# Optimization experiments

Hardware: AMD Instinct MI355X
Metric: run time of the kernel (lower is better)

Reference implementation:

```python
import jax, jax.numpy as jnp
import numpy as np

N = 20000
NNBR = 64
MESH = (64, 64, 64)
ORDER = 4          # B-spline interpolation order
ALPHA = 0.35       # Ewald splitting parameter (1/Angstrom)
BOX = 73.68        # cubic box edge (Angstrom)
KE = 14.399645478425668  # Coulomb constant, eV*Angstrom/e^2


def _Mn(x, n):
    """Cardinal B-spline M_n(x), support [0, n]."""
    if n == 2:
        return jnp.maximum(0.0, 1.0 - jnp.abs(x - 1.0))
    return (x * _Mn(x, n - 1) + (n - x) * _Mn(x - 1.0, n - 1)) / (n - 1)


def _bspline_fac(K):
    """|b(m)|^-2 ... i.e. 1/|Euler spline denominator|^2 per mesh dim."""
    m = jnp.arange(K, dtype=jnp.float32)
    k = jnp.arange(ORDER - 1, dtype=jnp.float32)
    Mv = _Mn(k + 1.0, ORDER)                       # M_n(1..n-1)
    phase = 2.0 * jnp.pi * m[:, None] * k[None, :] / K
    dre = jnp.sum(Mv * jnp.cos(phase), axis=1)
    dim = jnp.sum(Mv * jnp.sin(phase), axis=1)
    return 1.0 / (dre * dre + dim * dim)


def _pme_energy(positions, charges, cell, nbr, shifts):
    n = positions.shape[0]
    # ---------------- real-space short-range sum ----------------
    i_idx = jnp.arange(n)[:, None]
    valid = (nbr >= 0) & ~((nbr == i_idx) & jnp.all(shifts == 0, axis=-1))
    j = jnp.where(nbr >= 0, nbr, 0)
    rvec = positions[j] + shifts.astype(positions.dtype) @ cell - positions[:, None, :]
    r2 = jnp.sum(rvec * rvec, axis=-1)
    r = jnp.sqrt(jnp.where(valid, r2, 1.0))
    qq = charges[:, None] * charges[j]
    e_real = 0.5 * jnp.sum(jnp.where(valid, qq * jax.scipy.special.erfc(ALPHA * r) / r, 0.0))
    # ---------------- B-spline charge spreading ----------------
    Kx, Ky, Kz = MESH
    frac = positions @ jnp.linalg.inv(cell)        # cell rows = lattice vectors
    u = frac * jnp.array(MESH, dtype=positions.dtype)
    base = jnp.floor(u)
    t = u - base                                   # in [0, 1)
    basei = base.astype(jnp.int32)
    offs = jnp.arange(ORDER)
    wx = _Mn(t[:, 0:1] + offs, ORDER)              # [N, ORDER]
    wy = _Mn(t[:, 1:2] + offs, ORDER)
    wz = _Mn(t[:, 2:3] + offs, ORDER)
    ix = (basei[:, 0:1] - offs) % Kx
    iy = (basei[:, 1:2] - offs) % Ky
    iz = (basei[:, 2:3] - offs) % Kz
    W = (charges[:, None] * wx)[:, :, None, None] * wy[:, None, :, None] * wz[:, None, None, :]
    IDX = (ix[:, :, None, None] * Ky + iy[:, None, :, None]) * Kz + iz[:, None, None, :]
    mesh = jnp.zeros(Kx * Ky * Kz, positions.dtype).at[IDX.reshape(-1)].add(W.reshape(-1)).reshape(MESH)
    # ---------------- reciprocal-space FFT convolution ----------------
    Q = jnp.fft.fftn(mesh)
    Brec = 2.0 * jnp.pi * jnp.linalg.inv(cell).T   # rows are reciprocal vectors
    mx = (jnp.fft.fftfreq(Kx) * Kx).astype(positions.dtype)
    my = (jnp.fft.fftfreq(Ky) * Ky).astype(positions.dtype)
    mz = (jnp.fft.fftfreq(Kz) * Kz).astype(positions.dtype)
    kvec = (mx[:, None, None, None] * Brec[0] + my[None, :, None, None] * Brec[1]
            + mz[None, None, :, None] * Brec[2])
    k2 = jnp.sum(kvec * kvec, axis=-1)
    a2 = ALPHA * ALPHA
    kern = jnp.where(k2 > 0, jnp.exp(-k2 / (4.0 * a2)) / jnp.where(k2 > 0, k2, 1.0), 0.0)
    C = _bspline_fac(Kx)[:, None, None] * _bspline_fac(Ky)[None, :, None] * _bspline_fac(Kz)[None, None, :]
    vol = jnp.abs(jnp.linalg.det(cell))
    e_rec = (2.0 * jnp.pi / vol) * jnp.sum(kern * C * (Q.real ** 2 + Q.imag ** 2))
    # ---------------- self + neutralizing background ----------------
    qtot = jnp.sum(charges)
    e_self = -(ALPHA / jnp.sqrt(jnp.pi)) * jnp.sum(charges * charges)
    e_bg = -(jnp.pi / (2.0 * a2 * vol)) * qtot * qtot
    return e_real + e_rec + e_self + e_bg


def setup_inputs() -> dict:
    key = jax.random.key(0)
    k1, k2, k3 = jax.random.split(key, 3)
    positions = jax.random.uniform(k1, (N, 3), jnp.float32) * BOX
    q = jax.random.normal(k2, (N,), jnp.float32)
    q = q - jnp.mean(q)  # neutral system
    cell = BOX * jnp.eye(3, dtype=jnp.float32)
    nbr = jax.random.randint(k3, (N, NNBR), 0, N, jnp.int32)
    shifts = jnp.zeros((N, NNBR, 3), jnp.int32)
    return {"positions": positions, "node_charges": q, "cell": cell,
            "neighbor_matrix": nbr, "neighbor_shifts": shifts}


def reference(positions, node_charges, cell, neighbor_matrix, neighbor_shifts):
    def e_strain(pos, q, c, eps):
        F = jnp.eye(3, dtype=pos.dtype) + eps
        return _pme_energy(pos @ F, q, c @ F, neighbor_matrix, neighbor_shifts)

    eps0 = jnp.zeros((3, 3), positions.dtype)
    e, (g_pos, g_eps) = jax.value_and_grad(e_strain, argnums=(0, 3))(
        positions, node_charges, cell, eps0)
    vol = jnp.abs(jnp.linalg.det(cell))
    energies = e.reshape(1) * KE
    forces = -g_pos * KE
    virial = -0.5 * (g_eps + g_eps.T) * KE
    stresses = (virial / vol)[None]
    return energies, forces, stresses
```

## Files before the change

kernel.cpp:

```cpp
#include <hip/hip_runtime.h>
#include <math.h>

#define NATOM 20000
#define NNBR  64
#define KM    64
#define KM3   (KM*KM*KM)
#define NPAIR (NATOM*NNBR)

#define ALPHA_C 0.35f
#define KE_C    14.399645478425668f
#define TWO_OVER_SQRTPI 1.1283791670955126f
#define TWOPI_F 6.2831853071795864f
#define PI_F    3.14159265358979f
#define RC2     661.2244898f

#define WS_RE    0
#define WS_IM    (KM3)
#define WS_MESH  (2*KM3)
#define WS_GJ    (3*KM3)
#define WS_PART  (3*KM3 + 3*NATOM)
#define WS_FI    (WS_PART + 1024)
#define WS_POSQ  (WS_FI + 3*NATOM)
#define WS_NBS   (WS_POSQ + 4*NATOM)
#define ZERO_LEN (KM3 + 3*NATOM + 1024)

__device__ __forceinline__ float M2f(float x){ return fmaxf(0.f, 1.f - fabsf(x - 1.f)); }
__device__ __forceinline__ float M3f(float x){ return (x*M2f(x) + (3.f-x)*M2f(x-1.f)) * 0.5f; }
__device__ __forceinline__ float M4f(float x){ return (x*M3f(x) + (4.f-x)*M3f(x-1.f)) * (1.f/3.f); }

__device__ __forceinline__ float wsum64(float v){
#pragma unroll
  for(int off=32; off>0; off>>=1) v += __shfl_xor(v, off, 64);
  return v;
}

__device__ __forceinline__ float hinv9(const float* __restrict__ cell, float* h){
  float m00=cell[0],m01=cell[1],m02=cell[2];
  float m10=cell[3],m11=cell[4],m12=cell[5];
  float m20=cell[6],m21=cell[7],m22=cell[8];
  float det = m00*(m11*m22-m12*m21) - m01*(m10*m22-m12*m20) + m02*(m10*m21-m11*m20);
  float id = 1.f/det;
  h[0]=(m11*m22-m12*m21)*id; h[1]=(m02*m21-m01*m22)*id; h[2]=(m01*m12-m02*m11)*id;
  h[3]=(m12*m20-m10*m22)*id; h[4]=(m00*m22-m02*m20)*id; h[5]=(m02*m10-m00*m12)*id;
  h[6]=(m10*m21-m11*m20)*id; h[7]=(m01*m20-m00*m21)*id; h[8]=(m00*m11-m01*m10)*id;
  return fabsf(det);
}

__device__ __forceinline__ void fill_tw(int t, float* twr, float* twi){
  if(t < 64){
    float ss, cc; sincosf((TWOPI_F/64.f)*(float)t, &ss, &cc);
    twr[t] = cc; twi[t] = -ss;
  }
}

__device__ __forceinline__ void fft64t(float& xr, float& xi, int lane,
                                       const float* __restrict__ twr,
                                       const float* __restrict__ twi, float sgn){
#pragma unroll
  for(int k=0;k<6;k++){
    int half = 32 >> k;
    float or_ = __shfl_xor(xr, half, 64);
    float oi_ = __shfl_xor(xi, half, 64);
    bool hi = (lane & half) != 0;
    float sr = hi ? (or_ - xr) : (xr + or_);
    float si = hi ? (oi_ - xi) : (xi + oi_);
    int e = (lane & (half-1)) << k;
    float wr2 = hi ? twr[e] : 1.f;
    float wi2 = hi ? sgn*twi[e] : 0.f;
    xr = sr*wr2 - si*wi2;
    xi = sr*wi2 + si*wr2;
  }
  int rev = __brev((unsigned)lane) >> 26;
  xr = __shfl(xr, rev, 64);
  xi = __shfl(xi, rev, 64);
}

__global__ __launch_bounds__(256) void init_kernel(
    const float* __restrict__ pos, const float* __restrict__ q,
    const int* __restrict__ nbr, const int* __restrict__ shifts,
    float* __restrict__ zbase, float4* __restrict__ posq, int* __restrict__ nbs){
  int t = blockIdx.x*256 + threadIdx.x;
  if(t < ZERO_LEN) zbase[t] = 0.f;
  if(t < NATOM)
    posq[t] = make_float4(pos[3*t], pos[3*t+1], pos[3*t+2], q[t]);
  if(t < NPAIR){
    int j = nbr[t];
    int sx=shifts[3*t], sy=shifts[3*t+1], sz=shifts[3*t+2];
    int v;
    if(j < 0) v = -1;
    else v = (j & 0x7FFF) | ((sx+8)&15)<<15 | ((sy+8)&15)<<19 | ((sz+8)&15)<<23;
    nbs[t] = v;
  }
}

__global__ __launch_bounds__(256) void realspread_kernel(
    const float4* __restrict__ posq, const int* __restrict__ nbs,
    const float* __restrict__ cell,
    float* __restrict__ fi, float* __restrict__ gj, float* __restrict__ part,
    float* __restrict__ mesh){
  int lane = threadIdx.x & 63;
  int wid  = blockIdx.x*4 + (threadIdx.x>>6);
  float c0=cell[0],c1=cell[1],c2=cell[2];
  float c3=cell[3],c4=cell[4],c5=cell[5];
  float c6=cell[6],c7=cell[7],c8=cell[8];
  float h[9]; hinv9(cell, h);
  int la = lane>>4, lb = (lane>>2)&3, lc = lane&3;
  float e=0.f, vxx=0.f,vyy=0.f,vzz=0.f,vxy=0.f,vxz=0.f,vyz=0.f;
#pragma unroll
  for(int it=0; it<4; ++it){
    int i = wid*4 + it;
    float4 pi4 = posq[i];
    int v = nbs[i*NNBR + lane];
    {
      float u0=(pi4.x*h[0]+pi4.y*h[3]+pi4.z*h[6])*(float)KM;
      float u1=(pi4.x*h[1]+pi4.y*h[4]+pi4.z*h[7])*(float)KM;
      float u2=(pi4.x*h[2]+pi4.y*h[5]+pi4.z*h[8])*(float)KM;
      float b0=floorf(u0), b1=floorf(u1), b2=floorf(u2);
      float t0=u0-b0, t1=u1-b1, t2=u2-b2;
      int i0=(int)b0, i1=(int)b1, i2=(int)b2;
      float w = pi4.w * M4f(t0+(float)la) * M4f(t1+(float)lb) * M4f(t2+(float)lc);
      int ix=(i0-la+256)&63, iy=(i1-lb+256)&63, iz=(i2-lc+256)&63;
      unsafeAtomicAdd(&mesh[(ix*KM + iy)*KM + iz], w);
    }
    int j = v & 0x7FFF;
    int sx=((v>>15)&15)-8, sy=((v>>19)&15)-8, sz=((v>>23)&15)-8;
    bool self = (j==i) && (sx==0) && (sy==0) && (sz==0);
    float s=0.f, rx=0.f, ry=0.f, rz=0.f;
    if(v>=0 && !self){
      float4 pj = posq[j];
      rx = pj.x - pi4.x + sx*c0 + sy*c3 + sz*c6;
      ry = pj.y - pi4.y + sx*c1 + sy*c4 + sz*c7;
      rz = pj.z - pi4.z + sx*c2 + sy*c5 + sz*c8;
      float r2 = rx*rx + ry*ry + rz*rz;
      if(r2 > 0.f && r2 < RC2){
        float r = sqrtf(r2);
        float ar = ALPHA_C * r;
        float qq = pi4.w * pj.w;
        float ef = erfcf(ar);
        float ex = expf(-ar*ar);
        float ir = 1.f/r;
        e += 0.5f*qq*ef*ir;
        s  = 0.5f*qq*(ef + TWO_OVER_SQRTPI*ar*ex)*ir*ir*ir;
      }
    }
    float gx = s*rx, gy = s*ry, gz = s*rz;
    if(s != 0.f){
      unsafeAtomicAdd(&gj[3*j+0], -gx);
      unsafeAtomicAdd(&gj[3*j+1], -gy);
      unsafeAtomicAdd(&gj[3*j+2], -gz);
    }
    vxx -= s*rx*rx; vyy -= s*ry*ry; vzz -= s*rz*rz;
    vxy -= s*rx*ry; vxz -= s*rx*rz; vyz -= s*ry*rz;
    float tgx = wsum64(gx), tgy = wsum64(gy), tgz = wsum64(gz);
    if(lane==0){ fi[3*i]=tgx; fi[3*i+1]=tgy; fi[3*i+2]=tgz; }
  }
  e   = wsum64(e);
  vxx = wsum64(vxx); vyy = wsum64(vyy); vzz = wsum64(vzz);
  vxy = wsum64(vxy); vxz = wsum64(vxz); vyz = wsum64(vyz);
  if(lane==0){
    float* slot = part + (wid & 63)*16;
    unsafeAtomicAdd(&slot[0], e);
    unsafeAtomicAdd(&slot[1], vxx); unsafeAtomicAdd(&slot[2], vyy); unsafeAtomicAdd(&slot[3], vzz);
    unsafeAtomicAdd(&slot[4], vxy); unsafeAtomicAdd(&slot[5], vxz); unsafeAtomicAdd(&slot[6], vyz);
  }
}

__global__ __launch_bounds__(256) void fftZF(const float* __restrict__ mesh,
                                             float* __restrict__ re, float* __restrict__ im){
  __shared__ float twr[64], twi[64];
  int t = threadIdx.x, lane = t&63;
  fill_tw(t, twr, twi);
  __syncthreads();
  int idx = blockIdx.x*256 + t;
  float xr = mesh[idx], xi = 0.f;
  fft64t(xr, xi, lane, twr, twi, 1.f);
  re[idx]=xr; im[idx]=xi;
}

__global__ __launch_bounds__(256) void fftZI(float* __restrict__ re, const float* __restrict__ im){
  __shared__ float twr[64], twi[64];
  int t = threadIdx.x, lane = t&63;
  fill_tw(t, twr, twi);
  __syncthreads();
  int idx = blockIdx.x*256 + t;
  float xr = re[idx], xi = im[idx];
  fft64t(xr, xi, lane, twr, twi, -1.f);
  re[idx]=xr;
}

__global__ __launch_bounds__(256) void fftY(float* __restrict__ re, float* __restrict__ im,
                                            float sgn){
  __shared__ float lr[64][17], li[64][17], twr[64], twi[64];
  int t = threadIdx.x, lane = t&63, w = t>>6;
  fill_tw(t, twr, twi);
  int x = blockIdx.x>>2, z0 = (blockIdx.x&3)*16;
  int off = x*4096 + z0;
#pragma unroll
  for(int k=0;k<4;k++){
    int e = k*256 + t; int y = e>>4, zz = e&15;
    lr[y][zz] = re[off + y*64 + zz];
    li[y][zz] = im[off + y*64 + zz];
  }
  __syncthreads();
#pragma unroll
  for(int qq=0; qq<4; qq++){
    int zz = w*4 + qq;
    float xr = lr[lane][zz], xi = li[lane][zz];
    fft64t(xr, xi, lane, twr, twi, sgn);
    lr[lane][zz] = xr; li[lane][zz] = xi;
  }
  __syncthreads();
#pragma unroll
  for(int k=0;k<4;k++){
    int e = k*256 + t; int y = e>>4, zz = e&15;
    re[off + y*64 + zz] = lr[y][zz];
    im[off + y*64 + zz] = li[y][zz];
  }
}

__global__ __launch_bounds__(256) void fftB(float* __restrict__ re, float* __restrict__ im,
                                            const float* __restrict__ cell,
                                            float* __restrict__ part){
  __shared__ float lr[64][17], li[64][17], cf[64], twr[64], twi[64];
  int t = threadIdx.x, lane = t&63, w = t>>6;
  int y = blockIdx.x>>2, z0 = (blockIdx.x&3)*16;
  float h[9]; hinv9(cell, h);
  fill_tw(t, twr, twi);
  if(t < 64){
    float p1 = TWOPI_F*(float)t/64.f;
    float s1,c1_,s2,c2_; sincosf(p1,&s1,&c1_); sincosf(2.f*p1,&s2,&c2_);
    float dre = (1.f/6.f) + (2.f/3.f)*c1_ + (1.f/6.f)*c2_;
    float dim = (2.f/3.f)*s1 + (1.f/6.f)*s2;
    cf[t] = 1.f/(dre*dre + dim*dim);
  }
  float* rp = re + y*64 + z0;
  float* ip = im + y*64 + z0;
#pragma unroll
  for(int k=0;k<4;k++){
    int e = k*256 + t; int xI = e>>4, zz = e&15;
    lr[xI][zz] = rp[xI*4096 + zz];
    li[xI][zz] = ip[xI*4096 + zz];
  }
  __syncthreads();
  const float inv4a2 = 1.f/(4.f*ALPHA_C*ALPHA_C);
  float my_f = (float)((y<32)? y : y-64);
  float sE=0.f, v0=0.f,v1=0.f,v2=0.f,v3=0.f,v4=0.f,v5=0.f;
#pragma unroll
  for(int qq=0; qq<4; qq++){
    int zz = w*4 + qq; int z = z0 + zz;
    float xr = lr[lane][zz], xi = li[lane][zz];
    fft64t(xr, xi, lane, twr, twi, 1.f);
    int mx = lane, mz = z;
    float fx = (float)((mx<32)? mx : mx-64);
    float fz = (float)((mz<32)? mz : mz-64);
    float kx = TWOPI_F*(fx*h[0] + my_f*h[1] + fz*h[2]);
    float ky = TWOPI_F*(fx*h[3] + my_f*h[4] + fz*h[5]);
    float kz = TWOPI_F*(fx*h[6] + my_f*h[7] + fz*h[8]);
    float k2 = kx*kx + ky*ky + kz*kz;
    float wk = 0.f;
    if(k2 > 0.f){
      float kern = expf(-k2*inv4a2)/k2;
      wk = kern * cf[mx]*cf[y]*cf[z];
      float q2 = xr*xr + xi*xi;
      sE += wk*q2;
      float fac = wk*q2*(inv4a2 + 1.f/k2)*2.f;
      v0 += fac*kx*kx; v1 += fac*ky*ky; v2 += fac*kz*kz;
      v3 += fac*kx*ky; v4 += fac*kx*kz; v5 += fac*ky*kz;
    }
    lr[lane][zz] = wk*xr; li[lane][zz] = wk*xi;
  }
  __syncthreads();
#pragma unroll
  for(int k=0;k<4;k++){
    int e = k*256 + t; int xI = e>>4, zz = e&15;
    rp[xI*4096 + zz] = lr[xI][zz];
    ip[xI*4096 + zz] = li[xI][zz];
  }
  sE = wsum64(sE);
  v0 = wsum64(v0); v1 = wsum64(v1); v2 = wsum64(v2);
  v3 = wsum64(v3); v4 = wsum64(v4); v5 = wsum64(v5);
  if(lane==0){
    float* slot = part + (((blockIdx.x<<2)|w)&63)*16;
    unsafeAtomicAdd(&slot[7],  sE);
    unsafeAtomicAdd(&slot[8],  v0); unsafeAtomicAdd(&slot[9],  v1);
    unsafeAtomicAdd(&slot[10], v2); unsafeAtomicAdd(&slot[11], v3);
    unsafeAtomicAdd(&slot[12], v4); unsafeAtomicAdd(&slot[13], v5);
  }
}

__global__ __launch_bounds__(256) void fftC(float* __restrict__ re, float* __restrict__ im){
  __shared__ float lr[64][17], li[64][17], twr[64], twi[64];
  int t = threadIdx.x, lane = t&63, w = t>>6;
  fill_tw(t, twr, twi);
  int y = blockIdx.x>>2, z0 = (blockIdx.x&3)*16;
  float* rp = re + y*64 + z0;
  float* ip = im + y*64 + z0;
#pragma unroll
  for(int k=0;k<4;k++){
    int e = k*256 + t; int xI = e>>4, zz = e&15;
    lr[xI][zz] = rp[xI*4096 + zz];
    li[xI][zz] = ip[xI*4096 + zz];
  }
  __syncthreads();
#pragma unroll
  for(int qq=0; qq<4; qq++){
    int zz = w*4 + qq;
    float xr = lr[lane][zz], xi = li[lane][zz];
    fft64t(xr, xi, lane, twr, twi, -1.f);
    lr[lane][zz] = xr; li[lane][zz] = xi;
  }
  __syncthreads();
#pragma unroll
  for(int k=0;k<4;k++){
    int e = k*256 + t; int xI = e>>4, zz = e&15;
    rp[xI*4096 + zz] = lr[xI][zz];
    ip[xI*4096 + zz] = li[xI][zz];
  }
}

__global__ __launch_bounds__(256) void gather_kernel(
    const float4* __restrict__ posq, const float* __restrict__ cell,
    const float* __restrict__ phi,
    const float* __restrict__ fi, const float* __restrict__ gj,
    const float* __restrict__ part, float* __restrict__ out){
  __shared__ float sa[256], sb[256], facc[16];
  int wid  = blockIdx.x*4 + (threadIdx.x>>6);
  int lane = threadIdx.x & 63;
  float h[9]; float V = hinv9(cell, h);
  float4 pq = posq[wid];
  float u0=(pq.x*h[0]+pq.y*h[3]+pq.z*h[6])*(float)KM;
  float u1=(pq.x*h[1]+pq.y*h[4]+pq.z*h[7])*(float)KM;
  float u2=(pq.x*h[2]+pq.y*h[5]+pq.z*h[8])*(float)KM;
  float b0=floorf(u0), b1=floorf(u1), b2=floorf(u2);
  float t0=u0-b0, t1=u1-b1, t2=u2-b2;
  int i0=(int)b0, i1=(int)b1, i2=(int)b2;
  int a = lane>>4, b = (lane>>2)&3, c = lane&3;
  float fa=(float)a, fb=(float)b, fc=(float)c;
  float wxa=M4f(t0+fa), wyb=M4f(t1+fb), wzc=M4f(t2+fc);
  float dxa=M3f(t0+fa)-M3f(t0+fa-1.f);
  float dyb=M3f(t1+fb)-M3f(t1+fb-1.f);
  float dzc=M3f(t2+fc)-M3f(t2+fc-1.f);
  int ix=(i0-a+256)&63, iy=(i1-b+256)&63, iz=(i2-c+256)&63;
  float p = phi[(ix*KM + iy)*KM + iz];
  float Sx = wsum64(p*dxa*wyb*wzc);
  float Sy = wsum64(p*wxa*dyb*wzc);
  float Sz = wsum64(p*wxa*wyb*dzc);
  if(lane==0){
    float scale = pq.w * (2.f*TWOPI_F/V) * (float)KM;
    float g0 = scale*(Sx*h[0] + Sy*h[1] + Sz*h[2]);
    float g1 = scale*(Sx*h[3] + Sy*h[4] + Sz*h[5]);
    float g2 = scale*(Sx*h[6] + Sy*h[7] + Sz*h[8]);
    out[1+3*wid+0] = -KE_C*(fi[3*wid+0] + gj[3*wid+0] + g0);
    out[1+3*wid+1] = -KE_C*(fi[3*wid+1] + gj[3*wid+1] + g1);
    out[1+3*wid+2] = -KE_C*(fi[3*wid+2] + gj[3*wid+2] + g2);
  }
  if(blockIdx.x==0){
    int t = threadIdx.x;
    float qa=0.f, qb=0.f;
    for(int i=t;i<NATOM;i+=256){ float qv=posq[i].w; qa+=qv; qb+=qv*qv; }
    sa[t]=qa; sb[t]=qb; __syncthreads();
    for(int off=128; off>0; off>>=1){
      if(t<off){ sa[t]+=sa[t+off]; sb[t]+=sb[t+off]; } __syncthreads();
    }
    if(t<14){ float s=0.f; for(int sl=0;sl<64;sl++) s+=part[sl*16+t]; facc[t]=s; }
    __syncthreads();
    if(t==0){
      float qtot = sa[0], sumq2 = sb[0];
      float a2 = ALPHA_C*ALPHA_C;
      float pref = TWOPI_F/V;
      float e_real = facc[0];
      float e_rec  = pref*facc[7];
      float e_self = -(ALPHA_C/sqrtf(PI_F))*sumq2;
      float e_bg   = -(PI_F/(2.f*a2*V))*qtot*qtot;
      out[0] = (e_real + e_rec + e_self + e_bg)*KE_C;
      float gxx = facc[1] + pref*facc[8]  - e_rec - e_bg;
      float gyy = facc[2] + pref*facc[9]  - e_rec - e_bg;
      float gzz = facc[3] + pref*facc[10] - e_rec - e_bg;
      float gxy = facc[4] + pref*facc[11];
      float gxz = facc[5] + pref*facc[12];
      float gyz = facc[6] + pref*facc[13];
      float cc = -KE_C/V;
      float* st = out + 1 + 3*NATOM;
      st[0]=cc*gxx; st[4]=cc*gyy; st[8]=cc*gzz;
      st[1]=cc*gxy; st[3]=cc*gxy;
      st[2]=cc*gxz; st[6]=cc*gxz;
      st[5]=cc*gyz; st[7]=cc*gyz;
    }
  }
}

extern "C" void kernel_launch(void* const* d_in, const int* in_sizes, int n_in,
                              void* d_out, int out_size, void* d_ws, size_t ws_size,
                              hipStream_t stream) {
  const float* pos  = (const float*)d_in[0];
  const float* q    = (const float*)d_in[1];
  const float* cell = (const float*)d_in[2];
  const int* nbr    = (const int*)d_in[3];
  const int* shifts = (const int*)d_in[4];
  float* out = (float*)d_out;
  float* ws  = (float*)d_ws;
  float*  bufRe = ws + WS_RE;
  float*  bufIm = ws + WS_IM;
  float*  mesh  = ws + WS_MESH;
  float*  gj    = ws + WS_GJ;
  float*  part  = ws + WS_PART;
  float*  fi    = ws + WS_FI;
  float4* posq  = (float4*)(ws + WS_POSQ);
  int*    nbs   = (int*)(ws + WS_NBS);

  init_kernel<<<(NPAIR+255)/256,256,0,stream>>>(pos, q, nbr, shifts, mesh, posq, nbs);
  realspread_kernel<<<1250,256,0,stream>>>(posq, nbs, cell, fi, gj, part, mesh);
  fftZF<<<1024,256,0,stream>>>(mesh, bufRe, bufIm);
  fftY <<< 256,256,0,stream>>>(bufRe, bufIm, 1.f);
  fftB <<< 256,256,0,stream>>>(bufRe, bufIm, cell, part);
  fftC <<< 256,256,0,stream>>>(bufRe, bufIm);
  fftY <<< 256,256,0,stream>>>(bufRe, bufIm, -1.f);
  fftZI<<<1024,256,0,stream>>>(bufRe, bufIm);
  gather_kernel<<<5000,256,0,stream>>>(posq, cell, bufRe, fi, gj, part, out);
}
```

Before: 189.6 us.

## Fuse FFT stages into one cooperative kernel and split spreading from real-space pass

The six separate FFT and convolution launches are merged into a single cooperative kernel of 256 blocks, with grid-wide syncs between the Z, Y, X, and inverse stages. This removes several kernel launch gaps. The charge spreading moves out of the real-space kernel into its own 5000-block kernel with one atom per wavefront, so it no longer shares the real-space pair loop's per-iteration structure. In exchange, the Z-direction FFT now runs on only 256 blocks, each doing four passes, instead of 1024 blocks. It also adds grid-sync overhead and one extra launch for spreading.

```diff
diff --git a/kernel.cpp b/kernel.cpp
--- a/kernel.cpp
+++ b/kernel.cpp
@@ -1,5 +1,8 @@
 #include <hip/hip_runtime.h>
+#include <hip/hip_cooperative_groups.h>
 #include <math.h>
+
+namespace cg = cooperative_groups;
 
 #define NATOM 20000
 #define NNBR  64
@@ -93,35 +96,21 @@
   }
 }
 
-__global__ __launch_bounds__(256) void realspread_kernel(
+__global__ __launch_bounds__(256) void real_kernel(
     const float4* __restrict__ posq, const int* __restrict__ nbs,
     const float* __restrict__ cell,
-    float* __restrict__ fi, float* __restrict__ gj, float* __restrict__ part,
-    float* __restrict__ mesh){
+    float* __restrict__ fi, float* __restrict__ gj, float* __restrict__ part){
   int lane = threadIdx.x & 63;
   int wid  = blockIdx.x*4 + (threadIdx.x>>6);
   float c0=cell[0],c1=cell[1],c2=cell[2];
   float c3=cell[3],c4=cell[4],c5=cell[5];
   float c6=cell[6],c7=cell[7],c8=cell[8];
-  float h[9]; hinv9(cell, h);
-  int la = lane>>4, lb = (lane>>2)&3, lc = lane&3;
   float e=0.f, vxx=0.f,vyy=0.f,vzz=0.f,vxy=0.f,vxz=0.f,vyz=0.f;
 #pragma unroll
   for(int it=0; it<4; ++it){
     int i = wid*4 + it;
     float4 pi4 = posq[i];
     int v = nbs[i*NNBR + lane];
-    {
-      float u0=(pi4.x*h[0]+pi4.y*h[3]+pi4.z*h[6])*(float)KM;
-      float u1=(pi4.x*h[1]+pi4.y*h[4]+pi4.z*h[7])*(float)KM;
-      float u2=(pi4.x*h[2]+pi4.y*h[5]+pi4.z*h[8])*(float)KM;
-      float b0=floorf(u0), b1=floorf(u1), b2=floorf(u2);
-      float t0=u0-b0, t1=u1-b1, t2=u2-b2;
-      int i0=(int)b0, i1=(int)b1, i2=(int)b2;
-      float w = pi4.w * M4f(t0+(float)la) * M4f(t1+(float)lb) * M4f(t2+(float)lc);
-      int ix=(i0-la+256)&63, iy=(i1-lb+256)&63, iz=(i2-lc+256)&63;
-      unsafeAtomicAdd(&mesh[(ix*KM + iy)*KM + iz], w);
-    }
     int j = v & 0x7FFF;
     int sx=((v>>15)&15)-8, sy=((v>>19)&15)-8, sz=((v>>23)&15)-8;
     bool self = (j==i) && (sx==0) && (sy==0) && (sz==0);
@@ -165,66 +154,33 @@
   }
 }
 
-__global__ __launch_bounds__(256) void fftZF(const float* __restrict__ mesh,
-                                             float* __restrict__ re, float* __restrict__ im){
-  __shared__ float twr[64], twi[64];
-  int t = threadIdx.x, lane = t&63;
-  fill_tw(t, twr, twi);
-  __syncthreads();
-  int idx = blockIdx.x*256 + t;
-  float xr = mesh[idx], xi = 0.f;
-  fft64t(xr, xi, lane, twr, twi, 1.f);
-  re[idx]=xr; im[idx]=xi;
-}
-
-__global__ __launch_bounds__(256) void fftZI(float* __restrict__ re, const float* __restrict__ im){
-  __shared__ float twr[64], twi[64];
-  int t = threadIdx.x, lane = t&63;
-  fill_tw(t, twr, twi);
-  __syncthreads();
-  int idx = blockIdx.x*256 + t;
-  float xr = re[idx], xi = im[idx];
-  fft64t(xr, xi, lane, twr, twi, -1.f);
-  re[idx]=xr;
-}
-
-__global__ __launch_bounds__(256) void fftY(float* __restrict__ re, float* __restrict__ im,
-                                            float sgn){
-  __shared__ float lr[64][17], li[64][17], twr[64], twi[64];
+__global__ __launch_bounds__(256) void spread_kernel(
+    const float4* __restrict__ posq, const float* __restrict__ cell,
+    float* __restrict__ mesh){
+  int wid  = blockIdx.x*4 + (threadIdx.x>>6);
+  int lane = threadIdx.x & 63;
+  float h[9]; hinv9(cell, h);
+  float4 pq = posq[wid];
+  float u0=(pq.x*h[0]+pq.y*h[3]+pq.z*h[6])*(float)KM;
+  float u1=(pq.x*h[1]+pq.y*h[4]+pq.z*h[7])*(float)KM;
+  float u2=(pq.x*h[2]+pq.y*h[5]+pq.z*h[8])*(float)KM;
+  float b0=floorf(u0), b1=floorf(u1), b2=floorf(u2);
+  float t0=u0-b0, t1=u1-b1, t2=u2-b2;
+  int i0=(int)b0, i1=(int)b1, i2=(int)b2;
+  int a = lane>>4, b = (lane>>2)&3, c = lane&3;
+  float w = pq.w * M4f(t0+(float)a) * M4f(t1+(float)b) * M4f(t2+(float)c);
+  int ix=(i0-a+256)&63, iy=(i1-b+256)&63, iz=(i2-c+256)&63;
+  unsafeAtomicAdd(&mesh[(ix*KM + iy)*KM + iz], w);
+}
+
+__global__ __launch_bounds__(256) void fftAll(
+    float* __restrict__ re, float* __restrict__ im,
+    const float* __restrict__ mesh, const float* __restrict__ cell,
+    float* __restrict__ part){
+  cg::grid_group grid = cg::this_grid();
+  __shared__ float lr[64][17], li[64][17], twr[64], twi[64], cf[64];
   int t = threadIdx.x, lane = t&63, w = t>>6;
-  fill_tw(t, twr, twi);
-  int x = blockIdx.x>>2, z0 = (blockIdx.x&3)*16;
-  int off = x*4096 + z0;
-#pragma unroll
-  for(int k=0;k<4;k++){
-    int e = k*256 + t; int y = e>>4, zz = e&15;
-    lr[y][zz] = re[off + y*64 + zz];
-    li[y][zz] = im[off + y*64 + zz];
-  }
-  __syncthreads();
-#pragma unroll
-  for(int qq=0; qq<4; qq++){
-    int zz = w*4 + qq;
-    float xr = lr[lane][zz], xi = li[lane][zz];
-    fft64t(xr, xi, lane, twr, twi, sgn);
-    lr[lane][zz] = xr; li[lane][zz] = xi;
-  }
-  __syncthreads();
-#pragma unroll
-  for(int k=0;k<4;k++){
-    int e = k*256 + t; int y = e>>4, zz = e&15;
-    re[off + y*64 + zz] = lr[y][zz];
-    im[off + y*64 + zz] = li[y][zz];
-  }
-}
-
-__global__ __launch_bounds__(256) void fftB(float* __restrict__ re, float* __restrict__ im,
-                                            const float* __restrict__ cell,
-                                            float* __restrict__ part){
-  __shared__ float lr[64][17], li[64][17], cf[64], twr[64], twi[64];
-  int t = threadIdx.x, lane = t&63, w = t>>6;
-  int y = blockIdx.x>>2, z0 = (blockIdx.x&3)*16;
-  float h[9]; hinv9(cell, h);
+  int blk = blockIdx.x;
   fill_tw(t, twr, twi);
   if(t < 64){
     float p1 = TWOPI_F*(float)t/64.f;
@@ -233,88 +189,164 @@
     float dim = (2.f/3.f)*s1 + (1.f/6.f)*s2;
     cf[t] = 1.f/(dre*dre + dim*dim);
   }
-  float* rp = re + y*64 + z0;
-  float* ip = im + y*64 + z0;
+  __syncthreads();
+
 #pragma unroll
   for(int k=0;k<4;k++){
-    int e = k*256 + t; int xI = e>>4, zz = e&15;
-    lr[xI][zz] = rp[xI*4096 + zz];
-    li[xI][zz] = ip[xI*4096 + zz];
-  }
-  __syncthreads();
-  const float inv4a2 = 1.f/(4.f*ALPHA_C*ALPHA_C);
-  float my_f = (float)((y<32)? y : y-64);
-  float sE=0.f, v0=0.f,v1=0.f,v2=0.f,v3=0.f,v4=0.f,v5=0.f;
-#pragma unroll
-  for(int qq=0; qq<4; qq++){
-    int zz = w*4 + qq; int z = z0 + zz;
-    float xr = lr[lane][zz], xi = li[lane][zz];
+    int idx = blk*1024 + k*256 + t;
+    float xr = mesh[idx], xi = 0.f;
     fft64t(xr, xi, lane, twr, twi, 1.f);
-    int mx = lane, mz = z;
-    float fx = (float)((mx<32)? mx : mx-64);
-    float fz = (float)((mz<32)? mz : mz-64);
-    float kx = TWOPI_F*(fx*h[0] + my_f*h[1] + fz*h[2]);
-    float ky = TWOPI_F*(fx*h[3] + my_f*h[4] + fz*h[5]);
-    float kz = TWOPI_F*(fx*h[6] + my_f*h[7] + fz*h[8]);
-    float k2 = kx*kx + ky*ky + kz*kz;
-    float wk = 0.f;
-    if(k2 > 0.f){
-      float kern = expf(-k2*inv4a2)/k2;
-      wk = kern * cf[mx]*cf[y]*cf[z];
-      float q2 = xr*xr + xi*xi;
-      sE += wk*q2;
-      float fac = wk*q2*(inv4a2 + 1.f/k2)*2.f;
-      v0 += fac*kx*kx; v1 += fac*ky*ky; v2 += fac*kz*kz;
-      v3 += fac*kx*ky; v4 += fac*kx*kz; v5 += fac*ky*kz;
-    }
-    lr[lane][zz] = wk*xr; li[lane][zz] = wk*xi;
-  }
-  __syncthreads();
+    re[idx]=xr; im[idx]=xi;
+  }
+  grid.sync();
+
+  {
+    int x = blk>>2, z0 = (blk&3)*16;
+    int off = x*4096 + z0;
+#pragma unroll
+    for(int k=0;k<4;k++){
+      int e2 = k*256 + t; int y = e2>>4, zz = e2&15;
+      lr[y][zz] = re[off + y*64 + zz];
+      li[y][zz] = im[off + y*64 + zz];
+    }
+    __syncthreads();
+#pragma unroll
+    for(int qq=0; qq<4; qq++){
+      int zz = w*4 + qq;
+      float xr = lr[lane][zz], xi = li[lane][zz];
+      fft64t(xr, xi, lane, twr, twi, 1.f);
+      lr[lane][zz] = xr; li[lane][zz] = xi;
+    }
+    __syncthreads();
+#pragma unroll
+    for(int k=0;k<4;k++){
+      int e2 = k*256 + t; int y = e2>>4, zz = e2&15;
+      re[off + y*64 + zz] = lr[y][zz];
+      im[off + y*64 + zz] = li[y][zz];
+    }
+  }
+  grid.sync();
+
+  {
+    int y = blk>>2, z0 = (blk&3)*16;
+    float h[9]; hinv9(cell, h);
+    float* rp = re + y*64 + z0;
+    float* ip = im + y*64 + z0;
+#pragma unroll
+    for(int k=0;k<4;k++){
+      int e2 = k*256 + t; int xI = e2>>4, zz = e2&15;
+      lr[xI][zz] = rp[xI*4096 + zz];
+      li[xI][zz] = ip[xI*4096 + zz];
+    }
+    __syncthreads();
+    const float inv4a2 = 1.f/(4.f*ALPHA_C*ALPHA_C);
+    float my_f = (float)((y<32)? y : y-64);
+    float sE=0.f, v0=0.f,v1=0.f,v2=0.f,v3=0.f,v4=0.f,v5=0.f;
+#pragma unroll
+    for(int qq=0; qq<4; qq++){
+      int zz = w*4 + qq; int z = z0 + zz;
+      float xr = lr[lane][zz], xi = li[lane][zz];
+      fft64t(xr, xi, lane, twr, twi, 1.f);
+      int mx = lane, mz = z;
+      float fx = (float)((mx<32)? mx : mx-64);
+      float fz = (float)((mz<32)? mz : mz-64);
+      float kx = TWOPI_F*(fx*h[0] + my_f*h[1] + fz*h[2]);
+      float ky = TWOPI_F*(fx*h[3] + my_f*h[4] + fz*h[5]);
+      float kz = TWOPI_F*(fx*h[6] + my_f*h[7] + fz*h[8]);
+      float k2 = kx*kx + ky*ky + kz*kz;
+      float wk = 0.f;
+      if(k2 > 0.f){
+        float kern = expf(-k2*inv4a2)/k2;
+        wk = kern * cf[mx]*cf[y]*cf[z];
+        float q2 = xr*xr + xi*xi;
+        sE += wk*q2;
+        float fac = wk*q2*(inv4a2 + 1.f/k2)*2.f;
+        v0 += fac*kx*kx; v1 += fac*ky*ky; v2 += fac*kz*kz;
+        v3 += fac*kx*ky; v4 += fac*kx*kz; v5 += fac*ky*kz;
+      }
+      lr[lane][zz] = wk*xr; li[lane][zz] = wk*xi;
+    }
+    __syncthreads();
+#pragma unroll
+    for(int k=0;k<4;k++){
+      int e2 = k*256 + t; int xI = e2>>4, zz = e2&15;
+      rp[xI*4096 + zz] = lr[xI][zz];
+      ip[xI*4096 + zz] = li[xI][zz];
+    }
+    sE = wsum64(sE);
+    v0 = wsum64(v0); v1 = wsum64(v1); v2 = wsum64(v2);
+    v3 = wsum64(v3); v4 = wsum64(v4); v5 = wsum64(v5);
+    if(lane==0){
+      float* slot = part + (((blk<<2)|w)&63)*16;
+      unsafeAtomicAdd(&slot[7],  sE);
+      unsafeAtomicAdd(&slot[8],  v0); unsafeAtomicAdd(&slot[9],  v1);
+      unsafeAtomicAdd(&slot[10], v2); unsafeAtomicAdd(&slot[11], v3);
+      unsafeAtomicAdd(&slot[12], v4); unsafeAtomicAdd(&slot[13], v5);
+    }
+  }
+  grid.sync();
+
+  {
+    int y = blk>>2, z0 = (blk&3)*16;
+    float* rp = re + y*64 + z0;
+    float* ip = im + y*64 + z0;
+#pragma unroll
+    for(int k=0;k<4;k++){
+      int e2 = k*256 + t; int xI = e2>>4, zz = e2&15;
+      lr[xI][zz] = rp[xI*4096 + zz];
+      li[xI][zz] = ip[xI*4096 + zz];
+    }
+    __syncthreads();
+#pragma unroll
+    for(int qq=0; qq<4; qq++){
+      int zz = w*4 + qq;
+      float xr = lr[lane][zz], xi = li[lane][zz];
+      fft64t(xr, xi, lane, twr, twi, -1.f);
+      lr[lane][zz] = xr; li[lane][zz] = xi;
+    }
+    __syncthreads();
+#pragma unroll
+    for(int k=0;k<4;k++){
+      int e2 = k*256 + t; int xI = e2>>4, zz = e2&15;
+      rp[xI*4096 + zz] = lr[xI][zz];
+      ip[xI*4096 + zz] = li[xI][zz];
+    }
+  }
+  grid.sync();
+
+  {
+    int x = blk>>2, z0 = (blk&3)*16;
+    int off = x*4096 + z0;
+#pragma unroll
+    for(int k=0;k<4;k++){
+      int e2 = k*256 + t; int y = e2>>4, zz = e2&15;
+      lr[y][zz] = re[off + y*64 + zz];
+      li[y][zz] = im[off + y*64 + zz];
+    }
+    __syncthreads();
+#pragma unroll
+    for(int qq=0; qq<4; qq++){
+      int zz = w*4 + qq;
+      float xr = lr[lane][zz], xi = li[lane][zz];
+      fft64t(xr, xi, lane, twr, twi, -1.f);
+      lr[lane][zz] = xr; li[lane][zz] = xi;
+    }
+    __syncthreads();
+#pragma unroll
+    for(int k=0;k<4;k++){
+      int e2 = k*256 + t; int y = e2>>4, zz = e2&15;
+      re[off + y*64 + zz] = lr[y][zz];
+      im[off + y*64 + zz] = li[y][zz];
+    }
+  }
+  grid.sync();
+
 #pragma unroll
   for(int k=0;k<4;k++){
-    int e = k*256 + t; int xI = e>>4, zz = e&15;
-    rp[xI*4096 + zz] = lr[xI][zz];
-    ip[xI*4096 + zz] = li[xI][zz];
-  }
-  sE = wsum64(sE);
-  v0 = wsum64(v0); v1 = wsum64(v1); v2 = wsum64(v2);
-  v3 = wsum64(v3); v4 = wsum64(v4); v5 = wsum64(v5);
-  if(lane==0){
-    float* slot = part + (((blockIdx.x<<2)|w)&63)*16;
-    unsafeAtomicAdd(&slot[7],  sE);
-    unsafeAtomicAdd(&slot[8],  v0); unsafeAtomicAdd(&slot[9],  v1);
-    unsafeAtomicAdd(&slot[10], v2); unsafeAtomicAdd(&slot[11], v3);
-    unsafeAtomicAdd(&slot[12], v4); unsafeAtomicAdd(&slot[13], v5);
-  }
-}
-
-__global__ __launch_bounds__(256) void fftC(float* __restrict__ re, float* __restrict__ im){
-  __shared__ float lr[64][17], li[64][17], twr[64], twi[64];
-  int t = threadIdx.x, lane = t&63, w = t>>6;
-  fill_tw(t, twr, twi);
-  int y = blockIdx.x>>2, z0 = (blockIdx.x&3)*16;
-  float* rp = re + y*64 + z0;
-  float* ip = im + y*64 + z0;
-#pragma unroll
-  for(int k=0;k<4;k++){
-    int e = k*256 + t; int xI = e>>4, zz = e&15;
-    lr[xI][zz] = rp[xI*4096 + zz];
-    li[xI][zz] = ip[xI*4096 + zz];
-  }
-  __syncthreads();
-#pragma unroll
-  for(int qq=0; qq<4; qq++){
-    int zz = w*4 + qq;
-    float xr = lr[lane][zz], xi = li[lane][zz];
+    int idx = blk*1024 + k*256 + t;
+    float xr = re[idx], xi = im[idx];
     fft64t(xr, xi, lane, twr, twi, -1.f);
-    lr[lane][zz] = xr; li[lane][zz] = xi;
-  }
-  __syncthreads();
-#pragma unroll
-  for(int k=0;k<4;k++){
-    int e = k*256 + t; int xI = e>>4, zz = e&15;
-    rp[xI*4096 + zz] = lr[xI][zz];
-    ip[xI*4096 + zz] = li[xI][zz];
+    re[idx]=xr;
   }
 }
 
@@ -409,12 +441,12 @@
   int*    nbs   = (int*)(ws + WS_NBS);
 
   init_kernel<<<(NPAIR+255)/256,256,0,stream>>>(pos, q, nbr, shifts, mesh, posq, nbs);
-  realspread_kernel<<<1250,256,0,stream>>>(posq, nbs, cell, fi, gj, part, mesh);
-  fftZF<<<1024,256,0,stream>>>(mesh, bufRe, bufIm);
-  fftY <<< 256,256,0,stream>>>(bufRe, bufIm, 1.f);
-  fftB <<< 256,256,0,stream>>>(bufRe, bufIm, cell, part);
-  fftC <<< 256,256,0,stream>>>(bufRe, bufIm);
-  fftY <<< 256,256,0,stream>>>(bufRe, bufIm, -1.f);
-  fftZI<<<1024,256,0,stream>>>(bufRe, bufIm);
+  real_kernel<<<1250,256,0,stream>>>(posq, nbs, cell, fi, gj, part);
+  spread_kernel<<<5000,256,0,stream>>>(posq, cell, mesh);
+  {
+    const float* meshc = mesh;
+    void* args[] = { (void*)&bufRe, (void*)&bufIm, (void*)&meshc, (void*)&cell, (void*)&part };
+    hipLaunchCooperativeKernel((void*)fftAll, dim3(256), dim3(256), args, 0, stream);
+  }
   gather_kernel<<<5000,256,0,stream>>>(posq, cell, bufRe, fi, gj, part, out);
 }
```

Measured after the change: 348.2 us. +83.6%, slower.
